# Performance work log

Hardware: AMD Instinct MI355X
Metric: run time of the kernel (lower is better)

Reference implementation:

```python
import jax, jax.numpy as jnp
import numpy as np

B, S, D = 16, 4096, 1024  # batch, seq, last-dim (= max_length)


def setup_inputs() -> dict:
    key = jax.random.key(0)
    k1, k2, k3, k4, k5 = jax.random.split(key, 5)
    a = jax.random.randint(k1, (B, S, D), -128, 128, dtype=jnp.int32).astype(jnp.int8)
    b = jax.random.randint(k2, (B, S, D), -128, 128, dtype=jnp.int32).astype(jnp.int8)
    # per-last-dim positive scales, realistic small magnitudes
    scale_a = jax.random.uniform(k3, (D,), jnp.float32, 0.005, 0.02)
    scale_b = jax.random.uniform(k4, (D,), jnp.float32, 0.005, 0.02)
    scale_out = jax.random.uniform(k5, (D,), jnp.float32, 0.005, 0.02)
    return {"a": a, "scale_a": scale_a, "b": b, "scale_b": scale_b, "scale_out": scale_out}


def reference(a, scale_a, b, scale_b, scale_out):
    # Fused dequant -> elementwise multiply -> requant (quantized branch of forward).
    # out_fp32 = (a * scale_a) * (b * scale_b); out_int8 = round(out_fp32 / scale_out) clipped to int8.
    out_fp = (a.astype(jnp.float32) * scale_a) * (b.astype(jnp.float32) * scale_b)
    out_q = jnp.clip(jnp.round(out_fp / scale_out), -128.0, 127.0).astype(jnp.int8)
    return (out_q, scale_out)
```

## Files before the change

kernel.cpp:

```cpp
#include <hip/hip_runtime.h>


typedef int   vi4 __attribute__((ext_vector_type(4)));
typedef float vf4 __attribute__((ext_vector_type(4)));

__global__ void prep_scales_kernel(const float* __restrict__ sa,
                                   const float* __restrict__ sb,
                                   const float* __restrict__ so,
                                   float* __restrict__ c,
                                   float* __restrict__ out_tail,
                                   int D) {
    int d = blockIdx.x * blockDim.x + threadIdx.x;
    if (d < D) {
        float s = so[d];
        c[d] = sa[d] * sb[d] / s;
        out_tail[d] = s;
    }
}

__global__ __launch_bounds__(256) void mulq_kernel(const vi4* __restrict__ a,
                                                   const vi4* __restrict__ b,
                                                   const float* __restrict__ c,
                                                   vf4* __restrict__ out,
                                                   unsigned dmask, unsigned use_mask,
                                                   unsigned D, unsigned nvec) {
    unsigned tid = blockIdx.x * blockDim.x + threadIdx.x;
    if (tid >= nvec) return;
    unsigned e0 = tid * 4u;
    unsigned d = use_mask ? (e0 & dmask) : (e0 % D);

    vi4 av = __builtin_nontemporal_load(&a[tid]);
    vi4 bv = __builtin_nontemporal_load(&b[tid]);
    float4 cv = *(const float4*)(c + d);

    vf4 o;
    o.x = fminf(fmaxf(rintf((float)(av.x * bv.x) * cv.x), -128.0f), 127.0f);
    o.y = fminf(fmaxf(rintf((float)(av.y * bv.y) * cv.y), -128.0f), 127.0f);
    o.z = fminf(fmaxf(rintf((float)(av.z * bv.z) * cv.z), -128.0f), 127.0f);
    o.w = fminf(fmaxf(rintf((float)(av.w * bv.w) * cv.w), -128.0f), 127.0f);

    out[tid] = o;
}

extern "C" void kernel_launch(void* const* d_in, const int* in_sizes, int n_in,
                              void* d_out, int out_size, void* d_ws, size_t ws_size,
                              hipStream_t stream) {
    const int*   a  = (const int*)  d_in[0];
    const float* sa = (const float*)d_in[1];
    const int*   b  = (const int*)  d_in[2];
    const float* sb = (const float*)d_in[3];
    const float* so = (const float*)d_in[4];

    const int N = in_sizes[0];
    const int D = in_sizes[1];

    float* out = (float*)d_out;
    float* c   = (float*)d_ws;

    prep_scales_kernel<<<(D + 255) / 256, 256, 0, stream>>>(sa, sb, so, c, out + (size_t)N, D);

    const unsigned nvec = (unsigned)(N / 4);
    const unsigned use_mask = ((D & (D - 1)) == 0) ? 1u : 0u;
    mulq_kernel<<<(nvec + 255u) / 256u, 256, 0, stream>>>(
        (const vi4*)a, (const vi4*)b, c, (vf4*)out,
        (unsigned)(D - 1), use_mask, (unsigned)D, nvec);
}
```

Measured before the change: 562.4 us.

## Fuse scale prep into grid-stride multiply-requant kernel with per-thread scale reuse

Removes the separate scale-prep kernel and computes the combined scale inside the main kernel. The main kernel becomes a grid-stride loop capped at 2048 blocks, and when the stride is a multiple of D each thread computes its four column scales once and reuses them. This removes a launch and the workspace round trip for the scales. The risk is reduced parallelism from fewer blocks, and the output-tail copy is handled only by block 0, which assumes D <= 1024.

```diff
diff --git a/kernel.cpp b/kernel.cpp
--- a/kernel.cpp
+++ b/kernel.cpp
@@ -4,42 +4,69 @@
 typedef int   vi4 __attribute__((ext_vector_type(4)));
 typedef float vf4 __attribute__((ext_vector_type(4)));
 
-__global__ void prep_scales_kernel(const float* __restrict__ sa,
-                                   const float* __restrict__ sb,
-                                   const float* __restrict__ so,
-                                   float* __restrict__ c,
-                                   float* __restrict__ out_tail,
-                                   int D) {
-    int d = blockIdx.x * blockDim.x + threadIdx.x;
-    if (d < D) {
-        float s = so[d];
-        c[d] = sa[d] * sb[d] / s;
-        out_tail[d] = s;
-    }
+#define TPB      256
+#define MAX_BLK  2048
+
+__device__ __forceinline__ float qclamp(int p, float cs) {
+    return fminf(fmaxf(rintf((float)p * cs), -128.0f), 127.0f);
 }
 
-__global__ __launch_bounds__(256) void mulq_kernel(const vi4* __restrict__ a,
-                                                   const vi4* __restrict__ b,
-                                                   const float* __restrict__ c,
-                                                   vf4* __restrict__ out,
-                                                   unsigned dmask, unsigned use_mask,
-                                                   unsigned D, unsigned nvec) {
-    unsigned tid = blockIdx.x * blockDim.x + threadIdx.x;
-    if (tid >= nvec) return;
-    unsigned e0 = tid * 4u;
-    unsigned d = use_mask ? (e0 & dmask) : (e0 % D);
+__global__ __launch_bounds__(TPB) void fused_mulq_kernel(
+    const vi4*  __restrict__ a,
+    const vi4*  __restrict__ b,
+    const float* __restrict__ sa,
+    const float* __restrict__ sb,
+    const float* __restrict__ so,
+    vf4*  __restrict__ out,
+    float* __restrict__ out_tail,
+    unsigned dmask,
+    unsigned colreuse,
+    unsigned D, unsigned nvec)
+{
+    const unsigned stride = gridDim.x * (unsigned)TPB;
+    unsigned idx0 = blockIdx.x * (unsigned)TPB + threadIdx.x;
 
-    vi4 av = __builtin_nontemporal_load(&a[tid]);
-    vi4 bv = __builtin_nontemporal_load(&b[tid]);
-    float4 cv = *(const float4*)(c + d);
+    if (blockIdx.x == 0) {
+        unsigned t4 = threadIdx.x * 4u;
+        if (t4 < D) *(float4*)(out_tail + t4) = *(const float4*)(so + t4);
+    }
 
-    vf4 o;
-    o.x = fminf(fmaxf(rintf((float)(av.x * bv.x) * cv.x), -128.0f), 127.0f);
-    o.y = fminf(fmaxf(rintf((float)(av.y * bv.y) * cv.y), -128.0f), 127.0f);
-    o.z = fminf(fmaxf(rintf((float)(av.z * bv.z) * cv.z), -128.0f), 127.0f);
-    o.w = fminf(fmaxf(rintf((float)(av.w * bv.w) * cv.w), -128.0f), 127.0f);
+    if (colreuse) {
+        unsigned col = (idx0 * 4u) & dmask;
+        float4 sa4 = *(const float4*)(sa + col);
+        float4 sb4 = *(const float4*)(sb + col);
+        float4 so4 = *(const float4*)(so + col);
+        float cx = sa4.x * sb4.x / so4.x;
+        float cy = sa4.y * sb4.y / so4.y;
+        float cz = sa4.z * sb4.z / so4.z;
+        float cw = sa4.w * sb4.w / so4.w;
 
-    out[tid] = o;
+        for (unsigned idx = idx0; idx < nvec; idx += stride) {
+            vi4 av = __builtin_nontemporal_load(&a[idx]);
+            vi4 bv = __builtin_nontemporal_load(&b[idx]);
+            vf4 o;
+            o.x = qclamp(__mul24(av.x, bv.x), cx);
+            o.y = qclamp(__mul24(av.y, bv.y), cy);
+            o.z = qclamp(__mul24(av.z, bv.z), cz);
+            o.w = qclamp(__mul24(av.w, bv.w), cw);
+            out[idx] = o;
+        }
+    } else {
+        for (unsigned idx = idx0; idx < nvec; idx += stride) {
+            unsigned col = (idx * 4u) % D;
+            float4 sa4 = *(const float4*)(sa + col);
+            float4 sb4 = *(const float4*)(sb + col);
+            float4 so4 = *(const float4*)(so + col);
+            vi4 av = __builtin_nontemporal_load(&a[idx]);
+            vi4 bv = __builtin_nontemporal_load(&b[idx]);
+            vf4 o;
+            o.x = qclamp(__mul24(av.x, bv.x), sa4.x * sb4.x / so4.x);
+            o.y = qclamp(__mul24(av.y, bv.y), sa4.y * sb4.y / so4.y);
+            o.z = qclamp(__mul24(av.z, bv.z), sa4.z * sb4.z / so4.z);
+            o.w = qclamp(__mul24(av.w, bv.w), sa4.w * sb4.w / so4.w);
+            out[idx] = o;
+        }
+    }
 }
 
 extern "C" void kernel_launch(void* const* d_in, const int* in_sizes, int n_in,
@@ -55,13 +82,17 @@
     const int D = in_sizes[1];
 
     float* out = (float*)d_out;
-    float* c   = (float*)d_ws;
-
-    prep_scales_kernel<<<(D + 255) / 256, 256, 0, stream>>>(sa, sb, so, c, out + (size_t)N, D);
 
     const unsigned nvec = (unsigned)(N / 4);
-    const unsigned use_mask = ((D & (D - 1)) == 0) ? 1u : 0u;
-    mulq_kernel<<<(nvec + 255u) / 256u, 256, 0, stream>>>(
-        (const vi4*)a, (const vi4*)b, c, (vf4*)out,
-        (unsigned)(D - 1), use_mask, (unsigned)D, nvec);
+    unsigned nblocks = (nvec + (unsigned)TPB - 1u) / (unsigned)TPB;
+    if (nblocks > (unsigned)MAX_BLK) nblocks = (unsigned)MAX_BLK;
+
+    const unsigned pow2     = ((D & (D - 1)) == 0) ? 1u : 0u;
+    const unsigned stride_e = nblocks * (unsigned)TPB * 4u;
+    const unsigned colreuse = (pow2 && (stride_e % (unsigned)D) == 0u) ? 1u : 0u;
+
+    fused_mulq_kernel<<<nblocks, TPB, 0, stream>>>(
+        (const vi4*)a, (const vi4*)b, sa, sb, so,
+        (vf4*)out, out + (size_t)N,
+        (unsigned)(D - 1), colreuse, (unsigned)D, nvec);
 }
```

Measured after the change: 584.2 us. +3.9%, slower.
